# Performance work log

Hardware: AMD Instinct MI355X
Metric: run time of the kernel (lower is better)

The kernel has to match this reference:

```python
import jax, jax.numpy as jnp
import numpy as np

OUT = 16          # output_size
SCALE = 1.0 / 16.0  # 1/featmap_stride
GRID = 2          # sampling_ratio


def setup_inputs() -> dict:
    key = jax.random.key(0)
    k1, k2, k3 = jax.random.split(key, 3)
    N, C, T, H, W, K = 2, 256, 16, 56, 56, 5
    feat = jax.random.normal(k1, (N, C, T, H, W), jnp.float32)
    img = H * 16.0  # 896 px input image
    xy = jax.random.uniform(k2, (N, K, 2), minval=0.0, maxval=img - 300.0)
    wh = jax.random.uniform(k3, (N, K, 2), minval=32.0, maxval=290.0)
    boxes = jnp.concatenate([xy, xy + wh], axis=-1)  # valid xyxy boxes
    rois = jnp.concatenate([jnp.zeros((N, K, 1)), boxes], axis=-1).astype(jnp.float32)
    entity_mask = jnp.ones((N, 1, K, T), dtype=bool)  # unused by forward (as in original)
    return {"feat": feat, "rois": rois, "entity_mask": entity_mask}


def _roi_align_single(feat_n, boxes):
    """RoIAlign (aligned=True, avg pool, fixed sampling grid) for one clip.

    feat_n: (C, T, H, W) -- applied to every frame t at once.
    boxes:  (K, 4) xyxy in input-image coordinates.
    returns (T, K, C, OUT, OUT)
    """
    C, T, H, W = feat_n.shape
    K = boxes.shape[0]
    b = boxes * SCALE - 0.5  # aligned=True offset
    x1, y1, x2, y2 = b[:, 0], b[:, 1], b[:, 2], b[:, 3]
    bin_w = (x2 - x1) / OUT
    bin_h = (y2 - y1) / OUT
    g = (jnp.arange(GRID, dtype=feat_n.dtype) + 0.5) / GRID
    p = jnp.arange(OUT, dtype=feat_n.dtype)
    # sample coords per roi/bin/grid-point: (K, OUT, GRID)
    xs = x1[:, None, None] + (p[None, :, None] + g[None, None, :]) * bin_w[:, None, None]
    ys = y1[:, None, None] + (p[None, :, None] + g[None, None, :]) * bin_h[:, None, None]
    # full (K, OUT_h, OUT_w, GRID_h, GRID_w) coordinate grids
    Y = jnp.broadcast_to(ys[:, :, None, :, None], (K, OUT, OUT, GRID, GRID))
    X = jnp.broadcast_to(xs[:, None, :, None, :], (K, OUT, OUT, GRID, GRID))
    valid = (Y > -1.0) & (Y < H) & (X > -1.0) & (X < W)
    Yc = jnp.clip(Y, 0.0, H - 1.0)
    Xc = jnp.clip(X, 0.0, W - 1.0)
    y0 = jnp.floor(Yc).astype(jnp.int32)
    x0 = jnp.floor(Xc).astype(jnp.int32)
    y1i = jnp.minimum(y0 + 1, H - 1)
    x1i = jnp.minimum(x0 + 1, W - 1)
    ly = Yc - y0.astype(feat_n.dtype)
    lx = Xc - x0.astype(feat_n.dtype)
    hy = 1.0 - ly
    hx = 1.0 - lx
    m = valid.astype(feat_n.dtype)
    gat = lambda yi, xi: feat_n[:, :, yi, xi]  # -> (C, T, K, OUT, OUT, GRID, GRID)
    val = (gat(y0, x0) * (hy * hx * m)
           + gat(y0, x1i) * (hy * lx * m)
           + gat(y1i, x0) * (ly * hx * m)
           + gat(y1i, x1i) * (ly * lx * m))
    out = val.mean(axis=(-1, -2))  # avg over GRIDxGRID samples (mmcv divides by count)
    return out.transpose(1, 2, 0, 3, 4)  # (T, K, C, OUT, OUT)


def reference(feat, rois, entity_mask):
    # feat: (N, C, T, H, W); rois: (N, K, 5); entity_mask unused (as in original forward)
    boxes = rois[..., 1:5]
    roi_feats = jax.vmap(_roi_align_single)(feat, boxes)  # (N, T, K, C, OUT, OUT)
    return roi_feats, feat
```

## Files before the change

kernel.cpp:

```cpp
#include <hip/hip_runtime.h>

constexpr int N = 2, C = 256, T = 16, H = 56, W = 56, K = 5;
constexpr int ROI_TOTAL   = N * T * K * C * 16 * 16;
constexpr int FEAT_TOTAL  = N * C * T * H * W;
constexpr int COPY_BLOCKS = FEAT_TOTAL / 4 / 256;
constexpr int ROI_BLOCKS  = N * T * K * C;

constexpr int CHUNK = 129, ROI_PER_CHUNK = 80, COPY_PER_CHUNK = 49;
constexpr int TOTAL_BLOCKS = COPY_BLOCKS + ROI_BLOCKS;

constexpr int WMAX = 22;
constexpr int LDSW = 23;

__global__ __launch_bounds__(256) void fused_roi_copy_kernel(
    const float* __restrict__ feat,
    const float* __restrict__ rois,
    float* __restrict__ roi_out,
    float* __restrict__ feat_out)
{
    __shared__ float win[WMAX * LDSW];

    int chunk = blockIdx.x / CHUNK;
    int pos   = blockIdx.x - chunk * CHUNK;

    if (pos >= ROI_PER_CHUNK) {
        int i = (chunk * COPY_PER_CHUNK + (pos - ROI_PER_CHUNK)) * 256 + threadIdx.x;
        ((float4*)feat_out)[i] = ((const float4*)feat)[i];
        return;
    }

    int rb   = chunk * ROI_PER_CHUNK + pos;
    int c    = rb & 255;
    int rest = rb >> 8;
    int k  = rest % 5;
    int nt = rest / 5;
    int t  = nt & 15;
    int n  = nt >> 4;

    const float* r = rois + (n * K + k) * 5;
    float bx1 = r[1] * (1.0f / 16.0f) - 0.5f;
    float by1 = r[2] * (1.0f / 16.0f) - 0.5f;
    float bx2 = r[3] * (1.0f / 16.0f) - 0.5f;
    float by2 = r[4] * (1.0f / 16.0f) - 0.5f;
    float bw = (bx2 - bx1) * (1.0f / 16.0f);
    float bh = (by2 - by1) * (1.0f / 16.0f);

    float ymin = fminf(fmaxf(by1 + 0.25f  * bh, 0.0f), (float)(H - 1));
    float ymax = fminf(fmaxf(by1 + 15.75f * bh, 0.0f), (float)(H - 1));
    float xmin = fminf(fmaxf(bx1 + 0.25f  * bw, 0.0f), (float)(W - 1));
    float xmax = fminf(fmaxf(bx1 + 15.75f * bw, 0.0f), (float)(W - 1));
    int y_lo = (int)ymin;
    int x_lo = (int)xmin;
    int y_hi = min((int)ymax + 1, H - 1);
    int x_hi = min((int)xmax + 1, W - 1);
    int nrows = min(y_hi - y_lo + 1, WMAX);
    int ncols = min(x_hi - x_lo + 1, WMAX);

    const float* fp = feat + ((size_t)((n * C + c) * T + t)) * (H * W);

    {
        int cc = threadIdx.x & 31;
        for (int rr = threadIdx.x >> 5; rr < nrows; rr += 8) {
            if (cc < ncols)
                win[rr * LDSW + cc] = fp[(y_lo + rr) * W + x_lo + cc];
        }
    }
    __syncthreads();

    int px = threadIdx.x & 15;
    int py = threadIdx.x >> 4;

    float acc = 0.0f;
    #pragma unroll
    for (int gy = 0; gy < 2; ++gy) {
        float Yf = by1 + ((float)py + (gy ? 0.75f : 0.25f)) * bh;
        if (Yf > -1.0f && Yf < (float)H) {
            float Yc  = fminf(fmaxf(Yf, 0.0f), (float)(H - 1));
            int   y0  = (int)Yc;
            int   y1i = min(y0 + 1, H - 1);
            float ly  = Yc - (float)y0;
            float hy  = 1.0f - ly;
            const float* row0 = win + (y0  - y_lo) * LDSW;
            const float* row1 = win + (y1i - y_lo) * LDSW;
            #pragma unroll
            for (int gx = 0; gx < 2; ++gx) {
                float Xf = bx1 + ((float)px + (gx ? 0.75f : 0.25f)) * bw;
                if (Xf > -1.0f && Xf < (float)W) {
                    float Xc  = fminf(fmaxf(Xf, 0.0f), (float)(W - 1));
                    int   x0  = (int)Xc;
                    int   x1i = min(x0 + 1, W - 1);
                    float lx  = Xc - (float)x0;
                    float hx  = 1.0f - lx;
                    int   c0  = x0  - x_lo;
                    int   c1  = x1i - x_lo;
                    acc += (row0[c0] * hx + row0[c1] * lx) * hy
                         + (row1[c0] * hx + row1[c1] * lx) * ly;
                }
            }
        }
    }

    roi_out[rb * 256 + threadIdx.x] = acc * 0.25f;
}

extern "C" void kernel_launch(void* const* d_in, const int* in_sizes, int n_in,
                              void* d_out, int out_size, void* d_ws, size_t ws_size,
                              hipStream_t stream)
{
    const float* feat = (const float*)d_in[0];
    const float* rois = (const float*)d_in[1];

    float* roi_out  = (float*)d_out;
    float* feat_out = (float*)d_out + ROI_TOTAL;

    fused_roi_copy_kernel<<<TOTAL_BLOCKS, 256, 0, stream>>>(
        feat, rois, roi_out, feat_out);
}
```

Before: 245.1 us.

## Process four channels per ROI block with precomputed shared sampling weights

Each ROI block now handles four channels instead of one: each wavefront stages one channel's window into shared memory, and the bilinear offsets and weights are computed once into shared tables by 64 threads and reused across all four channels. The fused copy path and the ROI outputs now use nontemporal stores, and the block interleave ratio is adjusted to match the smaller ROI block count. This amortizes coordinate math and block scheduling overhead. In exchange it uses more shared memory per block and launches fewer ROI blocks, which may reduce parallelism and latency hiding.

```diff
diff --git a/kernel.cpp b/kernel.cpp
--- a/kernel.cpp
+++ b/kernel.cpp
@@ -1,16 +1,20 @@
 #include <hip/hip_runtime.h>
 
 constexpr int N = 2, C = 256, T = 16, H = 56, W = 56, K = 5;
+constexpr int CG = 4;
 constexpr int ROI_TOTAL   = N * T * K * C * 16 * 16;
 constexpr int FEAT_TOTAL  = N * C * T * H * W;
 constexpr int COPY_BLOCKS = FEAT_TOTAL / 4 / 256;
-constexpr int ROI_BLOCKS  = N * T * K * C;
+constexpr int ROI_BLOCKS  = N * T * K * (C / CG);
 
-constexpr int CHUNK = 129, ROI_PER_CHUNK = 80, COPY_PER_CHUNK = 49;
+constexpr int CHUNK = 69, ROI_PER_CHUNK = 20, COPY_PER_CHUNK = 49;
 constexpr int TOTAL_BLOCKS = COPY_BLOCKS + ROI_BLOCKS;
 
 constexpr int WMAX = 22;
 constexpr int LDSW = 23;
+constexpr int WSZ  = WMAX * LDSW;
+
+typedef float floatx4 __attribute__((ext_vector_type(4)));
 
 __global__ __launch_bounds__(256) void fused_roi_copy_kernel(
     const float* __restrict__ feat,
@@ -18,89 +22,114 @@
     float* __restrict__ roi_out,
     float* __restrict__ feat_out)
 {
-    __shared__ float win[WMAX * LDSW];
+    __shared__ float win[CG * WSZ];
+    __shared__ int   xoff[32], yoff[32];
+    __shared__ float xh[32], xl[32], yh[32], yl[32];
 
     int chunk = blockIdx.x / CHUNK;
     int pos   = blockIdx.x - chunk * CHUNK;
 
     if (pos >= ROI_PER_CHUNK) {
         int i = (chunk * COPY_PER_CHUNK + (pos - ROI_PER_CHUNK)) * 256 + threadIdx.x;
-        ((float4*)feat_out)[i] = ((const float4*)feat)[i];
+        floatx4 v = ((const floatx4*)feat)[i];
+        __builtin_nontemporal_store(v, ((floatx4*)feat_out) + i);
         return;
     }
 
     int rb   = chunk * ROI_PER_CHUNK + pos;
-    int c    = rb & 255;
-    int rest = rb >> 8;
+    int cg   = rb & 63;
+    int rest = rb >> 6;
     int k  = rest % 5;
     int nt = rest / 5;
     int t  = nt & 15;
     int n  = nt >> 4;
 
     const float* r = rois + (n * K + k) * 5;
-    float bx1 = r[1] * (1.0f / 16.0f) - 0.5f;
-    float by1 = r[2] * (1.0f / 16.0f) - 0.5f;
-    float bx2 = r[3] * (1.0f / 16.0f) - 0.5f;
-    float by2 = r[4] * (1.0f / 16.0f) - 0.5f;
-    float bw = (bx2 - bx1) * (1.0f / 16.0f);
-    float bh = (by2 - by1) * (1.0f / 16.0f);
+    float bx1 = r[1] * 0.0625f - 0.5f;
+    float by1 = r[2] * 0.0625f - 0.5f;
+    float bw  = (r[3] * 0.0625f - 0.5f - bx1) * 0.0625f;
+    float bh  = (r[4] * 0.0625f - 0.5f - by1) * 0.0625f;
 
+    float xmin = fminf(fmaxf(bx1 + 0.25f  * bw, 0.0f), (float)(W - 1));
+    float xmax = fminf(fmaxf(bx1 + 15.75f * bw, 0.0f), (float)(W - 1));
     float ymin = fminf(fmaxf(by1 + 0.25f  * bh, 0.0f), (float)(H - 1));
     float ymax = fminf(fmaxf(by1 + 15.75f * bh, 0.0f), (float)(H - 1));
-    float xmin = fminf(fmaxf(bx1 + 0.25f  * bw, 0.0f), (float)(W - 1));
-    float xmax = fminf(fmaxf(bx1 + 15.75f * bw, 0.0f), (float)(W - 1));
-    int y_lo = (int)ymin;
-    int x_lo = (int)xmin;
-    int y_hi = min((int)ymax + 1, H - 1);
-    int x_hi = min((int)xmax + 1, W - 1);
-    int nrows = min(y_hi - y_lo + 1, WMAX);
-    int ncols = min(x_hi - x_lo + 1, WMAX);
+    int x_lo = (int)xmin, y_lo = (int)ymin;
+    int ncx = min((int)xmax - x_lo + 2, WMAX);
+    int ncy = min((int)ymax - y_lo + 2, WMAX);
 
-    const float* fp = feat + ((size_t)((n * C + c) * T + t)) * (H * W);
+    int tid = threadIdx.x;
+
+    if (tid < 64) {
+        int  i   = tid & 31;
+        bool isY = tid >= 32;
+        int  p   = i >> 1, g = i & 1;
+        float b1  = isY ? by1 : bx1;
+        float bs  = isY ? bh  : bw;
+        float lim = (float)(isY ? H : W);
+        int   lo  = isY ? y_lo : x_lo;
+        float F  = b1 + ((float)p + (g ? 0.75f : 0.25f)) * bs;
+        float m  = (F > -1.0f && F < lim) ? 1.0f : 0.0f;
+        float Fc = fminf(fmaxf(F, 0.0f), lim - 1.0f);
+        int   f0 = (int)Fc;
+        float l  = Fc - (float)f0;
+        float h  = 1.0f - l;
+        if (isY) {
+            yoff[i] = (f0 - lo) * LDSW;
+            yh[i]   = h * m * 0.25f;
+            yl[i]   = l * m * 0.25f;
+        } else {
+            xoff[i] = f0 - lo;
+            xh[i]   = h * m;
+            xl[i]   = l * m;
+        }
+    }
 
     {
-        int cc = threadIdx.x & 31;
-        for (int rr = threadIdx.x >> 5; rr < nrows; rr += 8) {
-            if (cc < ncols)
-                win[rr * LDSW + cc] = fp[(y_lo + rr) * W + x_lo + cc];
+        int lane = tid & 63;
+        int wv   = __builtin_amdgcn_readfirstlane(tid >> 6);
+        int col  = lane & 31;
+        const float* fp = feat
+            + (size_t)(((n * C + (cg * CG + wv)) * T) + t) * (H * W);
+        float* wb = win + wv * WSZ;
+        int xg = min(x_lo + col, W - 1);
+        if (col < ncx) {
+            for (int rr = lane >> 5; rr < ncy; rr += 2) {
+                int y = min(y_lo + rr, H - 1);
+                wb[rr * LDSW + col] = fp[y * W + xg];
+            }
         }
     }
     __syncthreads();
 
-    int px = threadIdx.x & 15;
-    int py = threadIdx.x >> 4;
+    int px = tid & 15;
+    int py = tid >> 4;
 
-    float acc = 0.0f;
-    #pragma unroll
-    for (int gy = 0; gy < 2; ++gy) {
-        float Yf = by1 + ((float)py + (gy ? 0.75f : 0.25f)) * bh;
-        if (Yf > -1.0f && Yf < (float)H) {
-            float Yc  = fminf(fmaxf(Yf, 0.0f), (float)(H - 1));
-            int   y0  = (int)Yc;
-            int   y1i = min(y0 + 1, H - 1);
-            float ly  = Yc - (float)y0;
-            float hy  = 1.0f - ly;
-            const float* row0 = win + (y0  - y_lo) * LDSW;
-            const float* row1 = win + (y1i - y_lo) * LDSW;
-            #pragma unroll
-            for (int gx = 0; gx < 2; ++gx) {
-                float Xf = bx1 + ((float)px + (gx ? 0.75f : 0.25f)) * bw;
-                if (Xf > -1.0f && Xf < (float)W) {
-                    float Xc  = fminf(fmaxf(Xf, 0.0f), (float)(W - 1));
-                    int   x0  = (int)Xc;
-                    int   x1i = min(x0 + 1, W - 1);
-                    float lx  = Xc - (float)x0;
-                    float hx  = 1.0f - lx;
-                    int   c0  = x0  - x_lo;
-                    int   c1  = x1i - x_lo;
-                    acc += (row0[c0] * hx + row0[c1] * lx) * hy
-                         + (row1[c0] * hx + row1[c1] * lx) * ly;
-                }
-            }
-        }
+    int   xo0 = xoff[2 * px],     xo1 = xoff[2 * px + 1];
+    float hx0 = xh[2 * px],       lx0 = xl[2 * px];
+    float hx1 = xh[2 * px + 1],   lx1 = xl[2 * px + 1];
+    int   yo0 = yoff[2 * py],     yo1 = yoff[2 * py + 1];
+    float hy0 = yh[2 * py],       ly0 = yl[2 * py];
+    float hy1 = yh[2 * py + 1],   ly1 = yl[2 * py + 1];
+
+    int i00 = yo0 + xo0, i01 = yo0 + xo1;
+    int i10 = yo1 + xo0, i11 = yo1 + xo1;
+
+#define SAMP(idx, HY, LY, HX, LX)                                         \
+    ((HY) * ((HX) * wbc[(idx)] + (LX) * wbc[(idx) + 1]) +                 \
+     (LY) * ((HX) * wbc[(idx) + LDSW] + (LX) * wbc[(idx) + LDSW + 1]))
+
+    int obase = (rest * C + cg * CG) * 256 + tid;
+#pragma unroll
+    for (int cc = 0; cc < CG; ++cc) {
+        const float* wbc = win + cc * WSZ;
+        float acc = SAMP(i00, hy0, ly0, hx0, lx0)
+                  + SAMP(i01, hy0, ly0, hx1, lx1)
+                  + SAMP(i10, hy1, ly1, hx0, lx0)
+                  + SAMP(i11, hy1, ly1, hx1, lx1);
+        __builtin_nontemporal_store(acc, roi_out + obase + cc * 256);
     }
-
-    roi_out[rb * 256 + threadIdx.x] = acc * 0.25f;
+#undef SAMP
 }
 
 extern "C" void kernel_launch(void* const* d_in, const int* in_sizes, int n_in,
```

Result: faster. 223.0 us (-9.0%).

## Process one feature plane per block, reusing the loaded plane for copy and all ROIs

Applied to the files above, without the earlier changes.

Each block now loads an entire (n,c,t) feature plane once into registers, writes it out as the feature copy with nontemporal stores, and stages it into padded shared memory. All K boxes are then sampled from that shared copy. Before, the copy and the per-ROI window loads were separate blocks that each read the feature again. This is meant to cut duplicate global reads and to use streaming stores. In exchange the block needs more shared memory and the boundary handling is reworked into branchless masked weights.

```diff
diff --git a/kernel.cpp b/kernel.cpp
--- a/kernel.cpp
+++ b/kernel.cpp
@@ -1,106 +1,101 @@
 #include <hip/hip_runtime.h>
 
 constexpr int N = 2, C = 256, T = 16, H = 56, W = 56, K = 5;
-constexpr int ROI_TOTAL   = N * T * K * C * 16 * 16;
-constexpr int FEAT_TOTAL  = N * C * T * H * W;
-constexpr int COPY_BLOCKS = FEAT_TOTAL / 4 / 256;
-constexpr int ROI_BLOCKS  = N * T * K * C;
+constexpr int ROI_TOTAL  = N * T * K * C * 16 * 16;
+constexpr int FEAT_TOTAL = N * C * T * H * W;
+constexpr int PLANE  = H * W;
+constexpr int PV4    = PLANE / 4;
+constexpr int PW     = 60;
+constexpr int PLANES = N * C * T;
 
-constexpr int CHUNK = 129, ROI_PER_CHUNK = 80, COPY_PER_CHUNK = 49;
-constexpr int TOTAL_BLOCKS = COPY_BLOCKS + ROI_BLOCKS;
+typedef float floatx4 __attribute__((ext_vector_type(4)));
 
-constexpr int WMAX = 22;
-constexpr int LDSW = 23;
-
-__global__ __launch_bounds__(256) void fused_roi_copy_kernel(
+__global__ __launch_bounds__(256) void fused_plane_kernel(
     const float* __restrict__ feat,
     const float* __restrict__ rois,
     float* __restrict__ roi_out,
     float* __restrict__ feat_out)
 {
-    __shared__ float win[WMAX * LDSW];
+    __shared__ float win[H * PW];
 
-    int chunk = blockIdx.x / CHUNK;
-    int pos   = blockIdx.x - chunk * CHUNK;
+    int plane = blockIdx.x;
+    int t  = plane & 15;
+    int nc = plane >> 4;
+    int c  = nc & 255;
+    int n  = nc >> 8;
 
-    if (pos >= ROI_PER_CHUNK) {
-        int i = (chunk * COPY_PER_CHUNK + (pos - ROI_PER_CHUNK)) * 256 + threadIdx.x;
-        ((float4*)feat_out)[i] = ((const float4*)feat)[i];
-        return;
-    }
+    int tid = threadIdx.x;
 
-    int rb   = chunk * ROI_PER_CHUNK + pos;
-    int c    = rb & 255;
-    int rest = rb >> 8;
-    int k  = rest % 5;
-    int nt = rest / 5;
-    int t  = nt & 15;
-    int n  = nt >> 4;
+    const floatx4* src = (const floatx4*)feat + (size_t)plane * PV4;
+    floatx4*       dst = (floatx4*)feat_out   + (size_t)plane * PV4;
 
-    const float* r = rois + (n * K + k) * 5;
-    float bx1 = r[1] * (1.0f / 16.0f) - 0.5f;
-    float by1 = r[2] * (1.0f / 16.0f) - 0.5f;
-    float bx2 = r[3] * (1.0f / 16.0f) - 0.5f;
-    float by2 = r[4] * (1.0f / 16.0f) - 0.5f;
-    float bw = (bx2 - bx1) * (1.0f / 16.0f);
-    float bh = (by2 - by1) * (1.0f / 16.0f);
+    floatx4 v0 = src[tid];
+    floatx4 v1 = src[tid + 256];
+    floatx4 v2 = src[tid + 512];
+    floatx4 v3;
+    bool has4 = tid < (PV4 - 768);
+    if (has4) v3 = src[tid + 768];
 
-    float ymin = fminf(fmaxf(by1 + 0.25f  * bh, 0.0f), (float)(H - 1));
-    float ymax = fminf(fmaxf(by1 + 15.75f * bh, 0.0f), (float)(H - 1));
-    float xmin = fminf(fmaxf(bx1 + 0.25f  * bw, 0.0f), (float)(W - 1));
-    float xmax = fminf(fmaxf(bx1 + 15.75f * bw, 0.0f), (float)(W - 1));
-    int y_lo = (int)ymin;
-    int x_lo = (int)xmin;
-    int y_hi = min((int)ymax + 1, H - 1);
-    int x_hi = min((int)xmax + 1, W - 1);
-    int nrows = min(y_hi - y_lo + 1, WMAX);
-    int ncols = min(x_hi - x_lo + 1, WMAX);
+    __builtin_nontemporal_store(v0, dst + tid);
+    __builtin_nontemporal_store(v1, dst + tid + 256);
+    __builtin_nontemporal_store(v2, dst + tid + 512);
+    if (has4) __builtin_nontemporal_store(v3, dst + tid + 768);
 
-    const float* fp = feat + ((size_t)((n * C + c) * T + t)) * (H * W);
-
+    floatx4* wv4 = (floatx4*)win;
     {
-        int cc = threadIdx.x & 31;
-        for (int rr = threadIdx.x >> 5; rr < nrows; rr += 8) {
-            if (cc < ncols)
-                win[rr * LDSW + cc] = fp[(y_lo + rr) * W + x_lo + cc];
-        }
+        int j = tid;        int r = j / 14; wv4[r * 15 + (j - r * 14)] = v0;
+        j = tid + 256;      r = j / 14;     wv4[r * 15 + (j - r * 14)] = v1;
+        j = tid + 512;      r = j / 14;     wv4[r * 15 + (j - r * 14)] = v2;
+        if (has4) { j = tid + 768; r = j / 14; wv4[r * 15 + (j - r * 14)] = v3; }
     }
     __syncthreads();
 
-    int px = threadIdx.x & 15;
-    int py = threadIdx.x >> 4;
+    float pxf = (float)(tid & 15);
+    float pyf = (float)(tid >> 4);
+    int obase = (((n * T + t) * K) * C + c) * 256 + tid;
 
-    float acc = 0.0f;
+    auto axis = [](float F, int imax, int& i0, float& hw, float& lw) {
+        float lim = (float)(imax + 2);
+        float m   = (F > -1.0f && F < lim) ? 1.0f : 0.0f;
+        float Fc  = fminf(fmaxf(F, 0.0f), lim - 1.0f);
+        int   f0  = min((int)Fc, imax);
+        float l   = Fc - (float)f0;
+        hw = (1.0f - l) * m;
+        lw = l * m;
+        i0 = f0;
+    };
+
     #pragma unroll
-    for (int gy = 0; gy < 2; ++gy) {
-        float Yf = by1 + ((float)py + (gy ? 0.75f : 0.25f)) * bh;
-        if (Yf > -1.0f && Yf < (float)H) {
-            float Yc  = fminf(fmaxf(Yf, 0.0f), (float)(H - 1));
-            int   y0  = (int)Yc;
-            int   y1i = min(y0 + 1, H - 1);
-            float ly  = Yc - (float)y0;
-            float hy  = 1.0f - ly;
-            const float* row0 = win + (y0  - y_lo) * LDSW;
-            const float* row1 = win + (y1i - y_lo) * LDSW;
-            #pragma unroll
-            for (int gx = 0; gx < 2; ++gx) {
-                float Xf = bx1 + ((float)px + (gx ? 0.75f : 0.25f)) * bw;
-                if (Xf > -1.0f && Xf < (float)W) {
-                    float Xc  = fminf(fmaxf(Xf, 0.0f), (float)(W - 1));
-                    int   x0  = (int)Xc;
-                    int   x1i = min(x0 + 1, W - 1);
-                    float lx  = Xc - (float)x0;
-                    float hx  = 1.0f - lx;
-                    int   c0  = x0  - x_lo;
-                    int   c1  = x1i - x_lo;
-                    acc += (row0[c0] * hx + row0[c1] * lx) * hy
-                         + (row1[c0] * hx + row1[c1] * lx) * ly;
-                }
-            }
-        }
+    for (int k = 0; k < K; ++k) {
+        const float* rp = rois + (n * K + k) * 5;
+        float bx1 = rp[1] * 0.0625f - 0.5f;
+        float by1 = rp[2] * 0.0625f - 0.5f;
+        float bw  = (rp[3] * 0.0625f - 0.5f - bx1) * 0.0625f;
+        float bh  = (rp[4] * 0.0625f - 0.5f - by1) * 0.0625f;
+
+        int xa, xb, ya, yb;
+        float hxa, lxa, hxb, lxb, hya, lya, hyb, lyb;
+        axis(bx1 + (pxf + 0.25f) * bw, W - 2, xa, hxa, lxa);
+        axis(bx1 + (pxf + 0.75f) * bw, W - 2, xb, hxb, lxb);
+        axis(by1 + (pyf + 0.25f) * bh, H - 2, ya, hya, lya);
+        axis(by1 + (pyf + 0.75f) * bh, H - 2, yb, hyb, lyb);
+        hya *= 0.25f; lya *= 0.25f; hyb *= 0.25f; lyb *= 0.25f;
+
+        int iaa = ya * PW + xa, iab = ya * PW + xb;
+        int iba = yb * PW + xa, ibb = yb * PW + xb;
+
+#define SAMP(i, HY, LY, HX, LX)                                           \
+        ((HY) * ((HX) * win[(i)] + (LX) * win[(i) + 1]) +                 \
+         (LY) * ((HX) * win[(i) + PW] + (LX) * win[(i) + PW + 1]))
+
+        float acc = SAMP(iaa, hya, lya, hxa, lxa)
+                  + SAMP(iab, hya, lya, hxb, lxb)
+                  + SAMP(iba, hyb, lyb, hxa, lxa)
+                  + SAMP(ibb, hyb, lyb, hxb, lxb);
+#undef SAMP
+
+        __builtin_nontemporal_store(acc, roi_out + obase + k * (C * 256));
     }
-
-    roi_out[rb * 256 + threadIdx.x] = acc * 0.25f;
 }
 
 extern "C" void kernel_launch(void* const* d_in, const int* in_sizes, int n_in,
@@ -113,6 +108,6 @@
     float* roi_out  = (float*)d_out;
     float* feat_out = (float*)d_out + ROI_TOTAL;
 
-    fused_roi_copy_kernel<<<TOTAL_BLOCKS, 256, 0, stream>>>(
+    fused_plane_kernel<<<PLANES, 256, 0, stream>>>(
         feat, rois, roi_out, feat_out);
 }
```

After: 224.5 us. 8.4% less time.
